# Kernel tuning notes

Hardware: AMD Instinct MI355X
Metric: run time of the kernel (lower is better)

## Reference

```python
import jax, jax.numpy as jnp
import numpy as np

N, IN_DIM, H, K = 4096, 64, 64, 3
DT = 0.05


def graph_filter(z, S_powers, W):
    # z: [N, d_in], S_powers: [K, N, N], W: [K, d_in, d_out]
    zk = jnp.einsum('knm,md->knd', S_powers, z)   # K-hop diffused features
    return jnp.einsum('knd,kde->ne', zk, W)       # sum over taps k


def setup_inputs() -> dict:
    key = jax.random.key(0)
    ks = jax.random.split(key, 8)
    w_scale = 0.1
    return {
        'x': jax.random.normal(ks[0], (N, H), jnp.float32),
        'u': jax.random.normal(ks[1], (N, IN_DIM), jnp.float32),
        'S_powers': jax.random.normal(ks[2], (K, N, N), jnp.float32) / np.float32(np.sqrt(N)),
        'WA_hat': jax.random.normal(ks[3], (K, H, H), jnp.float32) * w_scale,
        'WB_hat': jax.random.normal(ks[4], (K, IN_DIM, H), jnp.float32) * w_scale,
        'WA_state': jax.random.normal(ks[5], (K, H, H), jnp.float32) * w_scale,
        'WB_state': jax.random.normal(ks[6], (K, IN_DIM, H), jnp.float32) * w_scale,
        'bx': jnp.zeros((1, H), jnp.float32),
        'bu': jnp.zeros((1, H), jnp.float32),
        'b': jnp.ones((1, H), jnp.float32) * 0.1,
        'n_steps': 4,
    }


def reference(x, u, S_powers, WA_hat, WB_hat, WA_state, WB_state, bx, bu, b, n_steps):
    # Input-driven terms are constant across solver steps; hoist them.
    fu = jax.nn.relu(graph_filter(u, S_powers, WB_hat) + bu)   # [N, H]
    sigma_c = jnp.tanh(graph_filter(u, S_powers, WB_state))    # [N, H]

    def step(xc, _):
        f = jax.nn.relu(graph_filter(xc, S_powers, WA_hat) + bx) + fu
        dx = -(b + f) * xc - graph_filter(xc, S_powers, WA_state) + f * sigma_c
        xn = jnp.clip(xc + DT * dx, -1.0, 1.0)
        return xn, None

    xf, _ = jax.lax.scan(step, x, None, length=n_steps)
    return xf
```

## Files before the change

### kernel.cpp

```cpp
#include <hip/hip_runtime.h>
#include <math.h>


typedef unsigned short u16;
typedef unsigned int u32;
typedef __attribute__((ext_vector_type(8))) short short8;
typedef __attribute__((ext_vector_type(4))) float f32x4;

#define NN 4096
#define HD 64
#define KB32 128
#define DT_C 0.05f

__device__ __forceinline__ u16 f2bf(float f) {
    u32 u = __float_as_uint(f);
    u += 0x7FFFu + ((u >> 16) & 1u);
    return (u16)(u >> 16);
}
__device__ __forceinline__ u32 pk2(float a, float b) {
    return (u32)f2bf(a) | ((u32)f2bf(b) << 16);
}

__global__ __launch_bounds__(256) void convS_kernel(
    const float* __restrict__ S, u16* __restrict__ SbT)
{
    const int slab = blockIdx.y;
    const int tap = slab >> 7, kb = slab & 127;
    const int t = threadIdx.x;
    const int n = blockIdx.x * 64 + (t >> 2);
    const int kq = (t & 3) * 8;
    const float* src = S + ((size_t)tap * NN + n) * NN + kb * 32 + kq;
    float4 f0 = ((const float4*)src)[0];
    float4 f1 = ((const float4*)src)[1];
    uint4 o;
    o.x = pk2(f0.x, f0.y); o.y = pk2(f0.z, f0.w);
    o.z = pk2(f1.x, f1.y); o.w = pk2(f1.z, f1.w);
    *(uint4*)(SbT + ((size_t)slab * NN + n) * 32 + kq) = o;
}

__global__ __launch_bounds__(256) void zprep_kernel(
    const float* __restrict__ u, const float* __restrict__ x,
    const float* __restrict__ WAh, const float* __restrict__ WAs,
    const float* __restrict__ WBh, const float* __restrict__ WBs,
    u16* __restrict__ utT, u16* __restrict__ xtT, u16* __restrict__ WtT)
{
    const int b = blockIdx.x;
    const int t = threadIdx.x;
    if (b < 256) {
        const float* z = (b < 128) ? u : x;
        u16* ztT = (b < 128) ? utT : xtT;
        const int kb = b & 127, n0 = kb * 32;
        __shared__ __align__(16) u16 tile[64][40];
        const int nl = t >> 3, c0 = (t & 7) * 8;
        const float* src = z + (size_t)(n0 + nl) * HD + c0;
        float4 f0 = ((const float4*)src)[0];
        float4 f1 = ((const float4*)src)[1];
        tile[c0 + 0][nl] = f2bf(f0.x); tile[c0 + 1][nl] = f2bf(f0.y);
        tile[c0 + 2][nl] = f2bf(f0.z); tile[c0 + 3][nl] = f2bf(f0.w);
        tile[c0 + 4][nl] = f2bf(f1.x); tile[c0 + 5][nl] = f2bf(f1.y);
        tile[c0 + 6][nl] = f2bf(f1.z); tile[c0 + 7][nl] = f2bf(f1.w);
        __syncthreads();
        const int e = t >> 2, kw0 = (t & 3) * 8;
        short8 v = *(const short8*)&tile[e][kw0];
        *(short8*)(ztT + ((size_t)kb * 64 + e) * 32 + kw0) = v;
    } else {
        for (int f = t; f < 4 * 6 * 64 * 32; f += 256) {
            int mat = f / 12288, r = f % 12288;
            int s = r / 2048, r2 = r % 2048;
            int e = r2 >> 5, kw = r2 & 31;
            int kp = s * 32 + kw, tap = kp >> 6, d = kp & 63;
            const float* Wm = (mat == 0) ? WAh : (mat == 1) ? WAs : (mat == 2) ? WBh : WBs;
            WtT[f] = f2bf(Wm[((size_t)tap * HD + d) * HD + e]);
        }
    }
}

__global__ __launch_bounds__(256) void pack_kernel(
    const float* __restrict__ xn, u16* __restrict__ xtT)
{
    const int kb = blockIdx.x, n0 = kb * 32;
    const int t = threadIdx.x;
    __shared__ __align__(16) u16 tile[64][40];
    const int nl = t >> 3, c0 = (t & 7) * 8;
    const float* src = xn + (size_t)(n0 + nl) * HD + c0;
    float4 f0 = ((const float4*)src)[0];
    float4 f1 = ((const float4*)src)[1];
    tile[c0 + 0][nl] = f2bf(f0.x); tile[c0 + 1][nl] = f2bf(f0.y);
    tile[c0 + 2][nl] = f2bf(f0.z); tile[c0 + 3][nl] = f2bf(f0.w);
    tile[c0 + 4][nl] = f2bf(f1.x); tile[c0 + 5][nl] = f2bf(f1.y);
    tile[c0 + 6][nl] = f2bf(f1.z); tile[c0 + 7][nl] = f2bf(f1.w);
    __syncthreads();
    const int e = t >> 2, kw0 = (t & 3) * 8;
    short8 v = *(const short8*)&tile[e][kw0];
    *(short8*)(xtT + ((size_t)kb * 64 + e) * 32 + kw0) = v;
}

__global__ __launch_bounds__(256) void diffuseA_kernel(
    const u16* __restrict__ SbT, const u16* __restrict__ utT,
    const u16* __restrict__ xtT, float* __restrict__ Yp, int iters)
{
    const int t = threadIdx.x;
    const int tap = blockIdx.z;
    const int row0 = blockIdx.x * 128;
    const int kb0 = blockIdx.y * iters;
    const int w = t >> 6, lane = t & 63, l15 = lane & 15, quad = lane >> 4;

    const u16* A0 = SbT + (((size_t)(tap * KB32) * NN + row0 + w * 32 + l15) * 32) + quad * 8;
    const size_t arowstride = (size_t)NN * 32;
    const u16* Bu = utT + (size_t)(l15)*0;

    f32x4 z4 = {0.f, 0.f, 0.f, 0.f};
    f32x4 acc[2][2][4];
    #pragma unroll
    for (int s = 0; s < 2; ++s)
        #pragma unroll
        for (int i = 0; i < 2; ++i)
            #pragma unroll
            for (int j = 0; j < 4; ++j) acc[s][i][j] = z4;

    #pragma unroll 2
    for (int it = 0; it < iters; ++it) {
        const int kb = kb0 + it;
        const u16* ab = A0 + (size_t)kb * arowstride;
        short8 a0 = *(const short8*)(ab);
        short8 a1 = *(const short8*)(ab + 16 * 32);
        #pragma unroll
        for (int ct = 0; ct < 4; ++ct) {
            const size_t bo = ((size_t)kb * 64 + ct * 16 + l15) * 32 + quad * 8;
            short8 bu = *(const short8*)(utT + bo);
            short8 bx = *(const short8*)(xtT + bo);
            acc[0][0][ct] = __builtin_amdgcn_mfma_f32_16x16x32_bf16(a0, bu, acc[0][0][ct], 0, 0, 0);
            acc[0][1][ct] = __builtin_amdgcn_mfma_f32_16x16x32_bf16(a1, bu, acc[0][1][ct], 0, 0, 0);
            acc[1][0][ct] = __builtin_amdgcn_mfma_f32_16x16x32_bf16(a0, bx, acc[1][0][ct], 0, 0, 0);
            acc[1][1][ct] = __builtin_amdgcn_mfma_f32_16x16x32_bf16(a1, bx, acc[1][1][ct], 0, 0, 0);
        }
    }
    (void)Bu;
    #pragma unroll
    for (int s = 0; s < 2; ++s) {
        float* yb = Yp + ((size_t)((blockIdx.y * 3 + tap) * 2 + s) * NN + row0) * HD;
        #pragma unroll
        for (int rt = 0; rt < 2; ++rt)
            #pragma unroll
            for (int ct = 0; ct < 4; ++ct)
                #pragma unroll
                for (int r = 0; r < 4; ++r)
                    yb[(size_t)(w * 32 + rt * 16 + quad * 4 + r) * HD + ct * 16 + l15] = acc[s][rt][ct][r];
    }
}

__global__ __launch_bounds__(256) void diffuseS_kernel(
    const u16* __restrict__ SbT, const u16* __restrict__ xtT,
    float* __restrict__ Yp, int iters)
{
    const int t = threadIdx.x;
    const int tap = blockIdx.z;
    const int row0 = blockIdx.x * 128;
    const int kb0 = blockIdx.y * iters;
    const int w = t >> 6, lane = t & 63, l15 = lane & 15, quad = lane >> 4;

    const u16* A0 = SbT + (((size_t)(tap * KB32) * NN + row0 + w * 32 + l15) * 32) + quad * 8;
    const size_t arowstride = (size_t)NN * 32;

    f32x4 z4 = {0.f, 0.f, 0.f, 0.f};
    f32x4 acc[2][4];
    #pragma unroll
    for (int i = 0; i < 2; ++i)
        #pragma unroll
        for (int j = 0; j < 4; ++j) acc[i][j] = z4;

    #pragma unroll 2
    for (int it = 0; it < iters; ++it) {
        const int kb = kb0 + it;
        const u16* ab = A0 + (size_t)kb * arowstride;
        short8 a0 = *(const short8*)(ab);
        short8 a1 = *(const short8*)(ab + 16 * 32);
        #pragma unroll
        for (int ct = 0; ct < 4; ++ct) {
            short8 bb = *(const short8*)(xtT + ((size_t)kb * 64 + ct * 16 + l15) * 32 + quad * 8);
            acc[0][ct] = __builtin_amdgcn_mfma_f32_16x16x32_bf16(a0, bb, acc[0][ct], 0, 0, 0);
            acc[1][ct] = __builtin_amdgcn_mfma_f32_16x16x32_bf16(a1, bb, acc[1][ct], 0, 0, 0);
        }
    }
    float* yb = Yp + ((size_t)(blockIdx.y * 3 + tap) * NN + row0) * HD;
    #pragma unroll
    for (int rt = 0; rt < 2; ++rt)
        #pragma unroll
        for (int ct = 0; ct < 4; ++ct)
            #pragma unroll
            for (int r = 0; r < 4; ++r)
                yb[(size_t)(w * 32 + rt * 16 + quad * 4 + r) * HD + ct * 16 + l15] = acc[rt][ct][r];
}

__global__ __launch_bounds__(256) void reduce_kernel(
    const float* __restrict__ Yp, int KS, int nsrc,
    u16* __restrict__ dst0, u16* __restrict__ dst1)
{
    const int tg = blockIdx.x * 256 + threadIdx.x;
    const int src = tg / 98304;
    const int r = tg - src * 98304;
    const int tap = r >> 15;
    const int r2 = r & 32767;
    const int n = r2 >> 3;
    const int dg = (r2 & 7) * 8;
    const float* p = Yp + (((size_t)tap * nsrc + src) * NN + n) * HD + dg;
    const size_t kstride = (size_t)3 * nsrc * NN * HD;
    float4 s0 = {0.f, 0.f, 0.f, 0.f}, s1 = {0.f, 0.f, 0.f, 0.f};
    for (int ks = 0; ks < KS; ++ks) {
        float4 v0 = ((const float4*)(p + ks * kstride))[0];
        float4 v1 = ((const float4*)(p + ks * kstride))[1];
        s0.x += v0.x; s0.y += v0.y; s0.z += v0.z; s0.w += v0.w;
        s1.x += v1.x; s1.y += v1.y; s1.z += v1.z; s1.w += v1.w;
    }
    u16* dst = src ? dst1 : dst0;
    uint4 o;
    o.x = pk2(s0.x, s0.y); o.y = pk2(s0.z, s0.w);
    o.z = pk2(s1.x, s1.y); o.w = pk2(s1.z, s1.w);
    *(uint4*)(dst + (((size_t)(tap * 2 + (dg >> 5)) * NN + n) * 32) + (dg & 31)) = o;
}

__global__ __launch_bounds__(64) void update_step_kernel(
    const u16* __restrict__ YxT, const u16* __restrict__ WtT,
    const float* __restrict__ bx, const float* __restrict__ bvec,
    const float* __restrict__ fu, const float* __restrict__ sc,
    const float* __restrict__ xc, float* __restrict__ xn)
{
    const int n0 = blockIdx.x * 16;
    const int lane = threadIdx.x, l15 = lane & 15, quad = lane >> 4;

    f32x4 z4 = {0.f, 0.f, 0.f, 0.f};
    f32x4 aF[4], aG[4];
    #pragma unroll
    for (int ct = 0; ct < 4; ++ct) { aF[ct] = z4; aG[ct] = z4; }
    #pragma unroll
    for (int s = 0; s < 6; ++s) {
        short8 a = *(const short8*)(YxT + (((size_t)s * NN + n0 + l15) * 32) + quad * 8);
        #pragma unroll
        for (int ct = 0; ct < 4; ++ct) {
            const size_t wo = (((size_t)(0 * 6 + s) * 64) + ct * 16 + l15) * 32 + quad * 8;
            short8 bF = *(const short8*)(WtT + wo);
            short8 bG = *(const short8*)(WtT + wo + 6 * 64 * 32);
            aF[ct] = __builtin_amdgcn_mfma_f32_16x16x32_bf16(a, bF, aF[ct], 0, 0, 0);
            aG[ct] = __builtin_amdgcn_mfma_f32_16x16x32_bf16(a, bG, aG[ct], 0, 0, 0);
        }
    }
    #pragma unroll
    for (int ct = 0; ct < 4; ++ct) {
        const int e = ct * 16 + l15;
        const float bxv = bx[e], bbv = bvec[e];
        #pragma unroll
        for (int r = 0; r < 4; ++r) {
            const int n = n0 + quad * 4 + r;
            const size_t o = (size_t)n * HD + e;
            float f = fmaxf(aF[ct][r] + bxv, 0.f) + fu[o];
            float g = aG[ct][r];
            float xv = xc[o];
            float dx = -(bbv + f) * xv - g + f * sc[o];
            xn[o] = fminf(fmaxf(xv + DT_C * dx, -1.f), 1.f);
        }
    }
}

__global__ __launch_bounds__(64) void update1_kernel(
    const u16* __restrict__ YuT, const u16* __restrict__ YxT,
    const u16* __restrict__ WtT,
    const float* __restrict__ bx, const float* __restrict__ bu,
    const float* __restrict__ bvec, const float* __restrict__ x0,
    float* __restrict__ fu, float* __restrict__ sc, float* __restrict__ x1)
{
    const int n0 = blockIdx.x * 16;
    const int lane = threadIdx.x, l15 = lane & 15, quad = lane >> 4;

    f32x4 z4 = {0.f, 0.f, 0.f, 0.f};
    f32x4 aFu[4], aSc[4], aF[4], aG[4];
    #pragma unroll
    for (int ct = 0; ct < 4; ++ct) { aFu[ct] = z4; aSc[ct] = z4; aF[ct] = z4; aG[ct] = z4; }
    #pragma unroll
    for (int s = 0; s < 6; ++s) {
        const size_t ao = (((size_t)s * NN + n0 + l15) * 32) + quad * 8;
        short8 au = *(const short8*)(YuT + ao);
        short8 ax = *(const short8*)(YxT + ao);
        #pragma unroll
        for (int ct = 0; ct < 4; ++ct) {
            const size_t wo = (((size_t)s * 64) + ct * 16 + l15) * 32 + quad * 8;
            short8 bF  = *(const short8*)(WtT + wo);
            short8 bG  = *(const short8*)(WtT + wo + 6 * 64 * 32);
            short8 bFu = *(const short8*)(WtT + wo + 2 * 6 * 64 * 32);
            short8 bSc = *(const short8*)(WtT + wo + 3 * 6 * 64 * 32);
            aF[ct]  = __builtin_amdgcn_mfma_f32_16x16x32_bf16(ax, bF,  aF[ct],  0, 0, 0);
            aG[ct]  = __builtin_amdgcn_mfma_f32_16x16x32_bf16(ax, bG,  aG[ct],  0, 0, 0);
            aFu[ct] = __builtin_amdgcn_mfma_f32_16x16x32_bf16(au, bFu, aFu[ct], 0, 0, 0);
            aSc[ct] = __builtin_amdgcn_mfma_f32_16x16x32_bf16(au, bSc, aSc[ct], 0, 0, 0);
        }
    }
    #pragma unroll
    for (int ct = 0; ct < 4; ++ct) {
        const int e = ct * 16 + l15;
        const float bxv = bx[e], buv = bu[e], bbv = bvec[e];
        #pragma unroll
        for (int r = 0; r < 4; ++r) {
            const int n = n0 + quad * 4 + r;
            const size_t o = (size_t)n * HD + e;
            float fuv = fmaxf(aFu[ct][r] + buv, 0.f);
            float scv = tanhf(aSc[ct][r]);
            float f = fmaxf(aF[ct][r] + bxv, 0.f) + fuv;
            float g = aG[ct][r];
            float xv = x0[o];
            float dx = -(bbv + f) * xv - g + f * scv;
            fu[o] = fuv; sc[o] = scv;
            x1[o] = fminf(fmaxf(xv + DT_C * dx, -1.f), 1.f);
        }
    }
}

extern "C" void kernel_launch(void* const* d_in, const int* in_sizes, int n_in,
                              void* d_out, int out_size, void* d_ws, size_t ws_size,
                              hipStream_t stream) {
    const float* x   = (const float*)d_in[0];
    const float* u   = (const float*)d_in[1];
    const float* S   = (const float*)d_in[2];
    const float* WAh = (const float*)d_in[3];
    const float* WBh = (const float*)d_in[4];
    const float* WAs = (const float*)d_in[5];
    const float* WBs = (const float*)d_in[6];
    const float* bx  = (const float*)d_in[7];
    const float* bu  = (const float*)d_in[8];
    const float* bvec= (const float*)d_in[9];
    float* out = (float*)d_out;

    const size_t sbf_bytes = (size_t)3 * NN * NN * 2;
    const size_t slice = (size_t)NN * HD * 4;
    const size_t rest = 2 * 524288 + 98304 + 2 * 1572864 + 4 * 1048576;
    int KS_A = 4, KS_S = 8;
    if (ws_size < sbf_bytes + 24 * slice + rest) { KS_A = 2; KS_S = 4; }
    if (ws_size < sbf_bytes + 12 * slice + rest) { KS_A = 1; KS_S = 2; }
    const int nslice = (KS_A * 6 > KS_S * 3) ? KS_A * 6 : KS_S * 3;

    char* p = (char*)d_ws;
    u16* SbT  = (u16*)p;         p += sbf_bytes;
    float* Yp = (float*)p;       p += (size_t)nslice * slice;
    u16* utT  = (u16*)p;         p += 524288;
    u16* xtT  = (u16*)p;         p += 524288;
    u16* WtT  = (u16*)p;         p += 98304;
    u16* YuT  = (u16*)p;         p += 1572864;
    u16* YxT  = (u16*)p;         p += 1572864;
    float* fu = (float*)p;       p += 1048576;
    float* sc = (float*)p;       p += 1048576;
    float* xA = (float*)p;       p += 1048576;
    float* xB = (float*)p;       p += 1048576;

    zprep_kernel<<<257, 256, 0, stream>>>(u, x, WAh, WAs, WBh, WBs, utT, xtT, WtT);
    convS_kernel<<<dim3(64, 384), 256, 0, stream>>>(S, SbT);

    diffuseA_kernel<<<dim3(32, KS_A, 3), 256, 0, stream>>>(SbT, utT, xtT, Yp, KB32 / KS_A);
    reduce_kernel<<<768, 256, 0, stream>>>(Yp, KS_A, 2, YuT, YxT);
    update1_kernel<<<256, 64, 0, stream>>>(YuT, YxT, WtT, bx, bu, bvec, x, fu, sc, xA);
    pack_kernel<<<128, 256, 0, stream>>>(xA, xtT);
    diffuseS_kernel<<<dim3(32, KS_S, 3), 256, 0, stream>>>(SbT, xtT, Yp, KB32 / KS_S);
    reduce_kernel<<<384, 256, 0, stream>>>(Yp, KS_S, 1, YxT, YxT);
    update_step_kernel<<<256, 64, 0, stream>>>(YxT, WtT, bx, bvec, fu, sc, xA, xB);
    pack_kernel<<<128, 256, 0, stream>>>(xB, xtT);

    diffuseS_kernel<<<dim3(32, KS_S, 3), 256, 0, stream>>>(SbT, xtT, Yp, KB32 / KS_S);
    reduce_kernel<<<384, 256, 0, stream>>>(Yp, KS_S, 1, YxT, YxT);
    update_step_kernel<<<256, 64, 0, stream>>>(YxT, WtT, bx, bvec, fu, sc, xB, xA);
    pack_kernel<<<128, 256, 0, stream>>>(xA, xtT);

    diffuseS_kernel<<<dim3(32, KS_S, 3), 256, 0, stream>>>(SbT, xtT, Yp, KB32 / KS_S);
    reduce_kernel<<<384, 256, 0, stream>>>(Yp, KS_S, 1, YxT, YxT);
    update_step_kernel<<<256, 64, 0, stream>>>(YxT, WtT, bx, bvec, fu, sc, xA, out);
}
```

Before: 533.4 us.

## Fuse all stages into one cooperative persistent kernel with grid syncs

Replaces the chain of about sixteen kernel launches (conversion, diffusion, reduction, update, pack) with a single cooperative kernel of 256 persistent blocks that runs each phase in turn, separated by grid-wide syncs. The split-K partial sums are now reduced inside the update phase, and the update writes the bf16 transposed state directly, so the separate reduce and pack kernels are gone. The diffusion loops also gain explicit register double-buffering of the next K-block's operands. The aim is to remove launch gaps and intermediate round trips, at the cost of a fixed grid of one block per CU at 256 threads, which may limit latency hiding in the memory-bound S conversion and diffusion phases.

New measurement: 815.1 us. 52.8% more time.

```diff
diff --git a/kernel.cpp b/kernel.cpp
--- a/kernel.cpp
+++ b/kernel.cpp
@@ -1,5 +1,8 @@
 #include <hip/hip_runtime.h>
+#include <hip/hip_cooperative_groups.h>
 #include <math.h>
+
+namespace cg = cooperative_groups;
 
 
 typedef unsigned short u16;
@@ -9,7 +12,6 @@
 
 #define NN 4096
 #define HD 64
-#define KB32 128
 #define DT_C 0.05f
 
 __device__ __forceinline__ u16 f2bf(float f) {
@@ -20,353 +22,398 @@
 __device__ __forceinline__ u32 pk2(float a, float b) {
     return (u32)f2bf(a) | ((u32)f2bf(b) << 16);
 }
-
-__global__ __launch_bounds__(256) void convS_kernel(
-    const float* __restrict__ S, u16* __restrict__ SbT)
-{
-    const int slab = blockIdx.y;
-    const int tap = slab >> 7, kb = slab & 127;
-    const int t = threadIdx.x;
-    const int n = blockIdx.x * 64 + (t >> 2);
-    const int kq = (t & 3) * 8;
-    const float* src = S + ((size_t)tap * NN + n) * NN + kb * 32 + kq;
-    float4 f0 = ((const float4*)src)[0];
-    float4 f1 = ((const float4*)src)[1];
-    uint4 o;
-    o.x = pk2(f0.x, f0.y); o.y = pk2(f0.z, f0.w);
-    o.z = pk2(f1.x, f1.y); o.w = pk2(f1.z, f1.w);
-    *(uint4*)(SbT + ((size_t)slab * NN + n) * 32 + kq) = o;
-}
-
-__global__ __launch_bounds__(256) void zprep_kernel(
-    const float* __restrict__ u, const float* __restrict__ x,
-    const float* __restrict__ WAh, const float* __restrict__ WAs,
-    const float* __restrict__ WBh, const float* __restrict__ WBs,
-    u16* __restrict__ utT, u16* __restrict__ xtT, u16* __restrict__ WtT)
-{
-    const int b = blockIdx.x;
-    const int t = threadIdx.x;
-    if (b < 256) {
-        const float* z = (b < 128) ? u : x;
-        u16* ztT = (b < 128) ? utT : xtT;
-        const int kb = b & 127, n0 = kb * 32;
-        __shared__ __align__(16) u16 tile[64][40];
-        const int nl = t >> 3, c0 = (t & 7) * 8;
-        const float* src = z + (size_t)(n0 + nl) * HD + c0;
-        float4 f0 = ((const float4*)src)[0];
-        float4 f1 = ((const float4*)src)[1];
-        tile[c0 + 0][nl] = f2bf(f0.x); tile[c0 + 1][nl] = f2bf(f0.y);
-        tile[c0 + 2][nl] = f2bf(f0.z); tile[c0 + 3][nl] = f2bf(f0.w);
-        tile[c0 + 4][nl] = f2bf(f1.x); tile[c0 + 5][nl] = f2bf(f1.y);
-        tile[c0 + 6][nl] = f2bf(f1.z); tile[c0 + 7][nl] = f2bf(f1.w);
-        __syncthreads();
-        const int e = t >> 2, kw0 = (t & 3) * 8;
-        short8 v = *(const short8*)&tile[e][kw0];
-        *(short8*)(ztT + ((size_t)kb * 64 + e) * 32 + kw0) = v;
-    } else {
-        for (int f = t; f < 4 * 6 * 64 * 32; f += 256) {
-            int mat = f / 12288, r = f % 12288;
-            int s = r / 2048, r2 = r % 2048;
-            int e = r2 >> 5, kw = r2 & 31;
-            int kp = s * 32 + kw, tap = kp >> 6, d = kp & 63;
-            const float* Wm = (mat == 0) ? WAh : (mat == 1) ? WAs : (mat == 2) ? WBh : WBs;
-            WtT[f] = f2bf(Wm[((size_t)tap * HD + d) * HD + e]);
-        }
-    }
-}
-
-__global__ __launch_bounds__(256) void pack_kernel(
-    const float* __restrict__ xn, u16* __restrict__ xtT)
-{
-    const int kb = blockIdx.x, n0 = kb * 32;
+__device__ __forceinline__ short8 pkfrag(const float4& a, const float4& b) {
+    union { short8 s; u32 w[4]; } r;
+    r.w[0] = pk2(a.x, a.y); r.w[1] = pk2(a.z, a.w);
+    r.w[2] = pk2(b.x, b.y); r.w[3] = pk2(b.z, b.w);
+    return r.s;
+}
+__device__ __forceinline__ void add4(float4& d, const float4& v) {
+    d.x += v.x; d.y += v.y; d.z += v.z; d.w += v.w;
+}
+#define MFMA __builtin_amdgcn_mfma_f32_16x16x32_bf16
+
+__device__ void prep_phase(const float* S, const float* u, const float* x0,
+                           const float* WAh, const float* WAs,
+                           const float* WBh, const float* WBs,
+                           u16* SbT, u16* utT, u16* xtT, u16* WtT)
+{
     const int t = threadIdx.x;
     __shared__ __align__(16) u16 tile[64][40];
-    const int nl = t >> 3, c0 = (t & 7) * 8;
-    const float* src = xn + (size_t)(n0 + nl) * HD + c0;
-    float4 f0 = ((const float4*)src)[0];
-    float4 f1 = ((const float4*)src)[1];
-    tile[c0 + 0][nl] = f2bf(f0.x); tile[c0 + 1][nl] = f2bf(f0.y);
-    tile[c0 + 2][nl] = f2bf(f0.z); tile[c0 + 3][nl] = f2bf(f0.w);
-    tile[c0 + 4][nl] = f2bf(f1.x); tile[c0 + 5][nl] = f2bf(f1.y);
-    tile[c0 + 6][nl] = f2bf(f1.z); tile[c0 + 7][nl] = f2bf(f1.w);
-    __syncthreads();
-    const int e = t >> 2, kw0 = (t & 3) * 8;
-    short8 v = *(const short8*)&tile[e][kw0];
-    *(short8*)(xtT + ((size_t)kb * 64 + e) * 32 + kw0) = v;
-}
-
-__global__ __launch_bounds__(256) void diffuseA_kernel(
-    const u16* __restrict__ SbT, const u16* __restrict__ utT,
-    const u16* __restrict__ xtT, float* __restrict__ Yp, int iters)
+    for (int uu = blockIdx.x; uu < 24576 + 257; uu += 256) {
+        if (uu < 24576) {
+            const int nx = uu & 63, slab = uu >> 6;
+            const int tap = slab >> 7, kb = slab & 127;
+            const int n = nx * 64 + (t >> 2), kq = (t & 3) * 8;
+            const float* src = S + ((size_t)tap * NN + n) * NN + kb * 32 + kq;
+            float4 f0 = ((const float4*)src)[0];
+            float4 f1 = ((const float4*)src)[1];
+            uint4 o;
+            o.x = pk2(f0.x, f0.y); o.y = pk2(f0.z, f0.w);
+            o.z = pk2(f1.x, f1.y); o.w = pk2(f1.z, f1.w);
+            *(uint4*)(SbT + ((size_t)slab * NN + n) * 32 + kq) = o;
+        } else if (uu < 24832) {
+            const int zu = uu - 24576;
+            const float* z = (zu < 128) ? u : x0;
+            u16* ztT = (zu < 128) ? utT : xtT;
+            const int kb = zu & 127, n0 = kb * 32;
+            const int nl = t >> 3, c0 = (t & 7) * 8;
+            const float* srcz = z + (size_t)(n0 + nl) * HD + c0;
+            float4 f0 = ((const float4*)srcz)[0];
+            float4 f1 = ((const float4*)srcz)[1];
+            tile[c0 + 0][nl] = f2bf(f0.x); tile[c0 + 1][nl] = f2bf(f0.y);
+            tile[c0 + 2][nl] = f2bf(f0.z); tile[c0 + 3][nl] = f2bf(f0.w);
+            tile[c0 + 4][nl] = f2bf(f1.x); tile[c0 + 5][nl] = f2bf(f1.y);
+            tile[c0 + 6][nl] = f2bf(f1.z); tile[c0 + 7][nl] = f2bf(f1.w);
+            __syncthreads();
+            const int e = t >> 2, kw0 = (t & 3) * 8;
+            short8 v = *(const short8*)&tile[e][kw0];
+            *(short8*)(ztT + ((size_t)kb * 64 + e) * 32 + kw0) = v;
+            __syncthreads();
+        } else {
+            for (int f = t; f < 4 * 6 * 64 * 32; f += 256) {
+                int mat = f / 12288, r = f % 12288;
+                int s = r / 2048, r2 = r % 2048;
+                int e = r2 >> 5, kw = r2 & 31;
+                int kp = s * 32 + kw, tap = kp >> 6, d = kp & 63;
+                const float* Wm = (mat == 0) ? WAh : (mat == 1) ? WAs
+                                 : (mat == 2) ? WBh : WBs;
+                WtT[f] = f2bf(Wm[((size_t)tap * HD + d) * HD + e]);
+            }
+        }
+    }
+}
+
+__device__ void diffuse_step_phase(const u16* SbT, const u16* xtT,
+                                   float* Yp, int KS)
 {
     const int t = threadIdx.x;
-    const int tap = blockIdx.z;
-    const int row0 = blockIdx.x * 128;
-    const int kb0 = blockIdx.y * iters;
     const int w = t >> 6, lane = t & 63, l15 = lane & 15, quad = lane >> 4;
-
-    const u16* A0 = SbT + (((size_t)(tap * KB32) * NN + row0 + w * 32 + l15) * 32) + quad * 8;
-    const size_t arowstride = (size_t)NN * 32;
-    const u16* Bu = utT + (size_t)(l15)*0;
-
-    f32x4 z4 = {0.f, 0.f, 0.f, 0.f};
-    f32x4 acc[2][2][4];
-    #pragma unroll
-    for (int s = 0; s < 2; ++s)
+    const int iters = 128 / KS;
+    for (int uu = blockIdx.x; uu < 96 * KS; uu += 256) {
+        const int rowblk = uu & 31;
+        const int tmp = uu >> 5;
+        const int ks = tmp % KS, tap = tmp / KS;
+        const int row0 = rowblk * 128;
+        const int slab0 = tap * 128 + ks * iters;
+        const int kb0 = ks * iters;
+        const u16* A0 = SbT + ((size_t)slab0 * NN + row0 + w * 32 + l15) * 32 + quad * 8;
+        const u16* B0 = xtT + ((size_t)kb0 * 64 + l15) * 32 + quad * 8;
+
+        f32x4 z4 = {0.f, 0.f, 0.f, 0.f};
+        f32x4 acc[2][4];
         #pragma unroll
         for (int i = 0; i < 2; ++i)
             #pragma unroll
-            for (int j = 0; j < 4; ++j) acc[s][i][j] = z4;
-
-    #pragma unroll 2
-    for (int it = 0; it < iters; ++it) {
-        const int kb = kb0 + it;
-        const u16* ab = A0 + (size_t)kb * arowstride;
-        short8 a0 = *(const short8*)(ab);
-        short8 a1 = *(const short8*)(ab + 16 * 32);
-        #pragma unroll
-        for (int ct = 0; ct < 4; ++ct) {
-            const size_t bo = ((size_t)kb * 64 + ct * 16 + l15) * 32 + quad * 8;
-            short8 bu = *(const short8*)(utT + bo);
-            short8 bx = *(const short8*)(xtT + bo);
-            acc[0][0][ct] = __builtin_amdgcn_mfma_f32_16x16x32_bf16(a0, bu, acc[0][0][ct], 0, 0, 0);
-            acc[0][1][ct] = __builtin_amdgcn_mfma_f32_16x16x32_bf16(a1, bu, acc[0][1][ct], 0, 0, 0);
-            acc[1][0][ct] = __builtin_amdgcn_mfma_f32_16x16x32_bf16(a0, bx, acc[1][0][ct], 0, 0, 0);
-            acc[1][1][ct] = __builtin_amdgcn_mfma_f32_16x16x32_bf16(a1, bx, acc[1][1][ct], 0, 0, 0);
-        }
-    }
-    (void)Bu;
-    #pragma unroll
-    for (int s = 0; s < 2; ++s) {
-        float* yb = Yp + ((size_t)((blockIdx.y * 3 + tap) * 2 + s) * NN + row0) * HD;
+            for (int j = 0; j < 4; ++j) acc[i][j] = z4;
+
+        short8 a0 = *(const short8*)(A0);
+        short8 a1 = *(const short8*)(A0 + 512);
+        short8 b0 = *(const short8*)(B0);
+        short8 b1 = *(const short8*)(B0 + 512);
+        short8 b2 = *(const short8*)(B0 + 1024);
+        short8 b3 = *(const short8*)(B0 + 1536);
+        for (int kb = 1; kb < iters; ++kb) {
+            const u16* An = A0 + (size_t)kb * (NN * 32);
+            const u16* Bn = B0 + (size_t)kb * 2048;
+            short8 na0 = *(const short8*)(An);
+            short8 na1 = *(const short8*)(An + 512);
+            short8 nb0 = *(const short8*)(Bn);
+            short8 nb1 = *(const short8*)(Bn + 512);
+            short8 nb2 = *(const short8*)(Bn + 1024);
+            short8 nb3 = *(const short8*)(Bn + 1536);
+            acc[0][0] = MFMA(a0, b0, acc[0][0], 0, 0, 0);
+            acc[1][0] = MFMA(a1, b0, acc[1][0], 0, 0, 0);
+            acc[0][1] = MFMA(a0, b1, acc[0][1], 0, 0, 0);
+            acc[1][1] = MFMA(a1, b1, acc[1][1], 0, 0, 0);
+            acc[0][2] = MFMA(a0, b2, acc[0][2], 0, 0, 0);
+            acc[1][2] = MFMA(a1, b2, acc[1][2], 0, 0, 0);
+            acc[0][3] = MFMA(a0, b3, acc[0][3], 0, 0, 0);
+            acc[1][3] = MFMA(a1, b3, acc[1][3], 0, 0, 0);
+            a0 = na0; a1 = na1; b0 = nb0; b1 = nb1; b2 = nb2; b3 = nb3;
+        }
+        acc[0][0] = MFMA(a0, b0, acc[0][0], 0, 0, 0);
+        acc[1][0] = MFMA(a1, b0, acc[1][0], 0, 0, 0);
+        acc[0][1] = MFMA(a0, b1, acc[0][1], 0, 0, 0);
+        acc[1][1] = MFMA(a1, b1, acc[1][1], 0, 0, 0);
+        acc[0][2] = MFMA(a0, b2, acc[0][2], 0, 0, 0);
+        acc[1][2] = MFMA(a1, b2, acc[1][2], 0, 0, 0);
+        acc[0][3] = MFMA(a0, b3, acc[0][3], 0, 0, 0);
+        acc[1][3] = MFMA(a1, b3, acc[1][3], 0, 0, 0);
+
+        float* yb = Yp + ((size_t)(ks * 3 + tap) * NN + row0) * HD;
         #pragma unroll
         for (int rt = 0; rt < 2; ++rt)
             #pragma unroll
             for (int ct = 0; ct < 4; ++ct)
                 #pragma unroll
                 for (int r = 0; r < 4; ++r)
-                    yb[(size_t)(w * 32 + rt * 16 + quad * 4 + r) * HD + ct * 16 + l15] = acc[s][rt][ct][r];
-    }
-}
-
-__global__ __launch_bounds__(256) void diffuseS_kernel(
-    const u16* __restrict__ SbT, const u16* __restrict__ xtT,
-    float* __restrict__ Yp, int iters)
+                    yb[(size_t)(w * 32 + rt * 16 + quad * 4 + r) * HD + ct * 16 + l15] =
+                        acc[rt][ct][r];
+    }
+}
+
+__device__ void diffuseA_phase(const u16* SbT, const u16* utT, const u16* xtT,
+                               float* Yp, int KS)
 {
     const int t = threadIdx.x;
-    const int tap = blockIdx.z;
-    const int row0 = blockIdx.x * 128;
-    const int kb0 = blockIdx.y * iters;
     const int w = t >> 6, lane = t & 63, l15 = lane & 15, quad = lane >> 4;
-
-    const u16* A0 = SbT + (((size_t)(tap * KB32) * NN + row0 + w * 32 + l15) * 32) + quad * 8;
-    const size_t arowstride = (size_t)NN * 32;
-
-    f32x4 z4 = {0.f, 0.f, 0.f, 0.f};
-    f32x4 acc[2][4];
-    #pragma unroll
-    for (int i = 0; i < 2; ++i)
+    const int iters = 128 / KS;
+    for (int uu = blockIdx.x; uu < 96 * KS; uu += 256) {
+        const int rowblk = uu & 31;
+        const int tmp = uu >> 5;
+        const int ks = tmp % KS, tap = tmp / KS;
+        const int row0 = rowblk * 128;
+        const int slab0 = tap * 128 + ks * iters;
+        const int kb0 = ks * iters;
+        const u16* A0 = SbT + ((size_t)slab0 * NN + row0 + w * 32 + l15) * 32 + quad * 8;
+        const size_t boff = ((size_t)kb0 * 64 + l15) * 32 + quad * 8;
+
+        f32x4 z4 = {0.f, 0.f, 0.f, 0.f};
+        f32x4 acc[2][2][4];
         #pragma unroll
-        for (int j = 0; j < 4; ++j) acc[i][j] = z4;
-
-    #pragma unroll 2
-    for (int it = 0; it < iters; ++it) {
-        const int kb = kb0 + it;
-        const u16* ab = A0 + (size_t)kb * arowstride;
-        short8 a0 = *(const short8*)(ab);
-        short8 a1 = *(const short8*)(ab + 16 * 32);
+        for (int s = 0; s < 2; ++s)
+            #pragma unroll
+            for (int i = 0; i < 2; ++i)
+                #pragma unroll
+                for (int j = 0; j < 4; ++j) acc[s][i][j] = z4;
+
+        short8 a0 = *(const short8*)(A0);
+        short8 a1 = *(const short8*)(A0 + 512);
+        short8 bu0 = *(const short8*)(utT + boff);
+        short8 bu1 = *(const short8*)(utT + boff + 512);
+        short8 bu2 = *(const short8*)(utT + boff + 1024);
+        short8 bu3 = *(const short8*)(utT + boff + 1536);
+        short8 bx0 = *(const short8*)(xtT + boff);
+        short8 bx1 = *(const short8*)(xtT + boff + 512);
+        short8 bx2 = *(const short8*)(xtT + boff + 1024);
+        short8 bx3 = *(const short8*)(xtT + boff + 1536);
+        for (int kb = 1; kb < iters; ++kb) {
+            const u16* An = A0 + (size_t)kb * (NN * 32);
+            const size_t bn = boff + (size_t)kb * 2048;
+            short8 na0 = *(const short8*)(An);
+            short8 na1 = *(const short8*)(An + 512);
+            short8 nu0 = *(const short8*)(utT + bn);
+            short8 nu1 = *(const short8*)(utT + bn + 512);
+            short8 nu2 = *(const short8*)(utT + bn + 1024);
+            short8 nu3 = *(const short8*)(utT + bn + 1536);
+            short8 nx0 = *(const short8*)(xtT + bn);
+            short8 nx1 = *(const short8*)(xtT + bn + 512);
+            short8 nx2 = *(const short8*)(xtT + bn + 1024);
+            short8 nx3 = *(const short8*)(xtT + bn + 1536);
+            acc[0][0][0] = MFMA(a0, bu0, acc[0][0][0], 0, 0, 0);
+            acc[0][1][0] = MFMA(a1, bu0, acc[0][1][0], 0, 0, 0);
+            acc[0][0][1] = MFMA(a0, bu1, acc[0][0][1], 0, 0, 0);
+            acc[0][1][1] = MFMA(a1, bu1, acc[0][1][1], 0, 0, 0);
+            acc[0][0][2] = MFMA(a0, bu2, acc[0][0][2], 0, 0, 0);
+            acc[0][1][2] = MFMA(a1, bu2, acc[0][1][2], 0, 0, 0);
+            acc[0][0][3] = MFMA(a0, bu3, acc[0][0][3], 0, 0, 0);
+            acc[0][1][3] = MFMA(a1, bu3, acc[0][1][3], 0, 0, 0);
+            acc[1][0][0] = MFMA(a0, bx0, acc[1][0][0], 0, 0, 0);
+            acc[1][1][0] = MFMA(a1, bx0, acc[1][1][0], 0, 0, 0);
+            acc[1][0][1] = MFMA(a0, bx1, acc[1][0][1], 0, 0, 0);
+            acc[1][1][1] = MFMA(a1, bx1, acc[1][1][1], 0, 0, 0);
+            acc[1][0][2] = MFMA(a0, bx2, acc[1][0][2], 0, 0, 0);
+            acc[1][1][2] = MFMA(a1, bx2, acc[1][1][2], 0, 0, 0);
+            acc[1][0][3] = MFMA(a0, bx3, acc[1][0][3], 0, 0, 0);
+            acc[1][1][3] = MFMA(a1, bx3, acc[1][1][3], 0, 0, 0);
+            a0 = na0; a1 = na1;
+            bu0 = nu0; bu1 = nu1; bu2 = nu2; bu3 = nu3;
+            bx0 = nx0; bx1 = nx1; bx2 = nx2; bx3 = nx3;
+        }
+        acc[0][0][0] = MFMA(a0, bu0, acc[0][0][0], 0, 0, 0);
+        acc[0][1][0] = MFMA(a1, bu0, acc[0][1][0], 0, 0, 0);
+        acc[0][0][1] = MFMA(a0, bu1, acc[0][0][1], 0, 0, 0);
+        acc[0][1][1] = MFMA(a1, bu1, acc[0][1][1], 0, 0, 0);
+        acc[0][0][2] = MFMA(a0, bu2, acc[0][0][2], 0, 0, 0);
+        acc[0][1][2] = MFMA(a1, bu2, acc[0][1][2], 0, 0, 0);
+        acc[0][0][3] = MFMA(a0, bu3, acc[0][0][3], 0, 0, 0);
+        acc[0][1][3] = MFMA(a1, bu3, acc[0][1][3], 0, 0, 0);
+        acc[1][0][0] = MFMA(a0, bx0, acc[1][0][0], 0, 0, 0);
+        acc[1][1][0] = MFMA(a1, bx0, acc[1][1][0], 0, 0, 0);
+        acc[1][0][1] = MFMA(a0, bx1, acc[1][0][1], 0, 0, 0);
+        acc[1][1][1] = MFMA(a1, bx1, acc[1][1][1], 0, 0, 0);
+        acc[1][0][2] = MFMA(a0, bx2, acc[1][0][2], 0, 0, 0);
+        acc[1][1][2] = MFMA(a1, bx2, acc[1][1][2], 0, 0, 0);
+        acc[1][0][3] = MFMA(a0, bx3, acc[1][0][3], 0, 0, 0);
+        acc[1][1][3] = MFMA(a1, bx3, acc[1][1][3], 0, 0, 0);
+
         #pragma unroll
-        for (int ct = 0; ct < 4; ++ct) {
-            short8 bb = *(const short8*)(xtT + ((size_t)kb * 64 + ct * 16 + l15) * 32 + quad * 8);
-            acc[0][ct] = __builtin_amdgcn_mfma_f32_16x16x32_bf16(a0, bb, acc[0][ct], 0, 0, 0);
-            acc[1][ct] = __builtin_amdgcn_mfma_f32_16x16x32_bf16(a1, bb, acc[1][ct], 0, 0, 0);
-        }
-    }
-    float* yb = Yp + ((size_t)(blockIdx.y * 3 + tap) * NN + row0) * HD;
-    #pragma unroll
-    for (int rt = 0; rt < 2; ++rt)
-        #pragma unroll
-        for (int ct = 0; ct < 4; ++ct)
+        for (int s = 0; s < 2; ++s) {
+            float* yb = Yp + ((size_t)((ks * 3 + tap) * 2 + s) * NN + row0) * HD;
             #pragma unroll
-            for (int r = 0; r < 4; ++r)
-                yb[(size_t)(w * 32 + rt * 16 + quad * 4 + r) * HD + ct * 16 + l15] = acc[rt][ct][r];
-}
-
-__global__ __launch_bounds__(256) void reduce_kernel(
-    const float* __restrict__ Yp, int KS, int nsrc,
-    u16* __restrict__ dst0, u16* __restrict__ dst1)
-{
-    const int tg = blockIdx.x * 256 + threadIdx.x;
-    const int src = tg / 98304;
-    const int r = tg - src * 98304;
-    const int tap = r >> 15;
-    const int r2 = r & 32767;
-    const int n = r2 >> 3;
-    const int dg = (r2 & 7) * 8;
-    const float* p = Yp + (((size_t)tap * nsrc + src) * NN + n) * HD + dg;
-    const size_t kstride = (size_t)3 * nsrc * NN * HD;
-    float4 s0 = {0.f, 0.f, 0.f, 0.f}, s1 = {0.f, 0.f, 0.f, 0.f};
-    for (int ks = 0; ks < KS; ++ks) {
-        float4 v0 = ((const float4*)(p + ks * kstride))[0];
-        float4 v1 = ((const float4*)(p + ks * kstride))[1];
-        s0.x += v0.x; s0.y += v0.y; s0.z += v0.z; s0.w += v0.w;
-        s1.x += v1.x; s1.y += v1.y; s1.z += v1.z; s1.w += v1.w;
-    }
-    u16* dst = src ? dst1 : dst0;
-    uint4 o;
-    o.x = pk2(s0.x, s0.y); o.y = pk2(s0.z, s0.w);
-    o.z = pk2(s1.x, s1.y); o.w = pk2(s1.z, s1.w);
-    *(uint4*)(dst + (((size_t)(tap * 2 + (dg >> 5)) * NN + n) * 32) + (dg & 31)) = o;
-}
-
-__global__ __launch_bounds__(64) void update_step_kernel(
-    const u16* __restrict__ YxT, const u16* __restrict__ WtT,
-    const float* __restrict__ bx, const float* __restrict__ bvec,
-    const float* __restrict__ fu, const float* __restrict__ sc,
-    const float* __restrict__ xc, float* __restrict__ xn)
-{
+            for (int rt = 0; rt < 2; ++rt)
+                #pragma unroll
+                for (int ct = 0; ct < 4; ++ct)
+                    #pragma unroll
+                    for (int r = 0; r < 4; ++r)
+                        yb[(size_t)(w * 32 + rt * 16 + quad * 4 + r) * HD + ct * 16 + l15] =
+                            acc[s][rt][ct][r];
+        }
+    }
+}
+
+__device__ void update_step_phase(const float* Yp, int KS, const u16* WtT,
+                                  const float* bx, const float* bvec,
+                                  const float* fu, const float* sc,
+                                  const float* xc, float* xn, u16* xtT)
+{
+    const int t = threadIdx.x;
+    const int w = t >> 6, lane = t & 63, l15 = lane & 15, quad = lane >> 4;
     const int n0 = blockIdx.x * 16;
-    const int lane = threadIdx.x, l15 = lane & 15, quad = lane >> 4;
-
-    f32x4 z4 = {0.f, 0.f, 0.f, 0.f};
-    f32x4 aF[4], aG[4];
-    #pragma unroll
-    for (int ct = 0; ct < 4; ++ct) { aF[ct] = z4; aG[ct] = z4; }
+    f32x4 aF = {0.f, 0.f, 0.f, 0.f}, aG = aF;
     #pragma unroll
     for (int s = 0; s < 6; ++s) {
-        short8 a = *(const short8*)(YxT + (((size_t)s * NN + n0 + l15) * 32) + quad * 8);
-        #pragma unroll
-        for (int ct = 0; ct < 4; ++ct) {
-            const size_t wo = (((size_t)(0 * 6 + s) * 64) + ct * 16 + l15) * 32 + quad * 8;
-            short8 bF = *(const short8*)(WtT + wo);
-            short8 bG = *(const short8*)(WtT + wo + 6 * 64 * 32);
-            aF[ct] = __builtin_amdgcn_mfma_f32_16x16x32_bf16(a, bF, aF[ct], 0, 0, 0);
-            aG[ct] = __builtin_amdgcn_mfma_f32_16x16x32_bf16(a, bG, aG[ct], 0, 0, 0);
-        }
-    }
+        const float* base = Yp + ((size_t)(s >> 1) * NN + n0 + l15) * HD
+                               + (s & 1) * 32 + quad * 8;
+        float4 p0 = {0.f, 0.f, 0.f, 0.f}, p1 = p0;
+        for (int ks = 0; ks < KS; ++ks) {
+            const float* pp = base + (size_t)ks * 3 * NN * HD;
+            add4(p0, ((const float4*)pp)[0]);
+            add4(p1, ((const float4*)pp)[1]);
+        }
+        short8 a = pkfrag(p0, p1);
+        const size_t wo = ((size_t)s * 64 + w * 16 + l15) * 32 + quad * 8;
+        short8 bF = *(const short8*)(WtT + wo);
+        short8 bG = *(const short8*)(WtT + wo + 12288);
+        aF = MFMA(a, bF, aF, 0, 0, 0);
+        aG = MFMA(a, bG, aG, 0, 0, 0);
+    }
+    const int e = w * 16 + l15;
+    const float bxv = bx[e], bbv = bvec[e];
     #pragma unroll
-    for (int ct = 0; ct < 4; ++ct) {
-        const int e = ct * 16 + l15;
-        const float bxv = bx[e], bbv = bvec[e];
-        #pragma unroll
-        for (int r = 0; r < 4; ++r) {
-            const int n = n0 + quad * 4 + r;
-            const size_t o = (size_t)n * HD + e;
-            float f = fmaxf(aF[ct][r] + bxv, 0.f) + fu[o];
-            float g = aG[ct][r];
-            float xv = xc[o];
-            float dx = -(bbv + f) * xv - g + f * sc[o];
-            xn[o] = fminf(fmaxf(xv + DT_C * dx, -1.f), 1.f);
-        }
-    }
-}
-
-__global__ __launch_bounds__(64) void update1_kernel(
-    const u16* __restrict__ YuT, const u16* __restrict__ YxT,
-    const u16* __restrict__ WtT,
-    const float* __restrict__ bx, const float* __restrict__ bu,
-    const float* __restrict__ bvec, const float* __restrict__ x0,
-    float* __restrict__ fu, float* __restrict__ sc, float* __restrict__ x1)
-{
+    for (int r = 0; r < 4; ++r) {
+        const int n = n0 + quad * 4 + r;
+        const size_t o = (size_t)n * HD + e;
+        float f = fmaxf(aF[r] + bxv, 0.f) + fu[o];
+        float xv = xc[o];
+        float dx = -(bbv + f) * xv - aG[r] + f * sc[o];
+        float xnv = fminf(fmaxf(xv + DT_C * dx, -1.f), 1.f);
+        xn[o] = xnv;
+        xtT[((size_t)(n >> 5) * 64 + e) * 32 + (n & 31)] = f2bf(xnv);
+    }
+}
+
+__device__ void update1_phase(const float* Yp, int KS, const u16* WtT,
+                              const float* bx, const float* bu, const float* bvec,
+                              const float* x0, float* fu, float* sc,
+                              float* xn, u16* xtT)
+{
+    const int t = threadIdx.x;
+    const int w = t >> 6, lane = t & 63, l15 = lane & 15, quad = lane >> 4;
     const int n0 = blockIdx.x * 16;
-    const int lane = threadIdx.x, l15 = lane & 15, quad = lane >> 4;
-
-    f32x4 z4 = {0.f, 0.f, 0.f, 0.f};
-    f32x4 aFu[4], aSc[4], aF[4], aG[4];
-    #pragma unroll
-    for (int ct = 0; ct < 4; ++ct) { aFu[ct] = z4; aSc[ct] = z4; aF[ct] = z4; aG[ct] = z4; }
+    f32x4 aF = {0.f, 0.f, 0.f, 0.f}, aG = aF, aFu = aF, aSc = aF;
     #pragma unroll
     for (int s = 0; s < 6; ++s) {
-        const size_t ao = (((size_t)s * NN + n0 + l15) * 32) + quad * 8;
-        short8 au = *(const short8*)(YuT + ao);
-        short8 ax = *(const short8*)(YxT + ao);
-        #pragma unroll
-        for (int ct = 0; ct < 4; ++ct) {
-            const size_t wo = (((size_t)s * 64) + ct * 16 + l15) * 32 + quad * 8;
-            short8 bF  = *(const short8*)(WtT + wo);
-            short8 bG  = *(const short8*)(WtT + wo + 6 * 64 * 32);
-            short8 bFu = *(const short8*)(WtT + wo + 2 * 6 * 64 * 32);
-            short8 bSc = *(const short8*)(WtT + wo + 3 * 6 * 64 * 32);
-            aF[ct]  = __builtin_amdgcn_mfma_f32_16x16x32_bf16(ax, bF,  aF[ct],  0, 0, 0);
-            aG[ct]  = __builtin_amdgcn_mfma_f32_16x16x32_bf16(ax, bG,  aG[ct],  0, 0, 0);
-            aFu[ct] = __builtin_amdgcn_mfma_f32_16x16x32_bf16(au, bFu, aFu[ct], 0, 0, 0);
-            aSc[ct] = __builtin_amdgcn_mfma_f32_16x16x32_bf16(au, bSc, aSc[ct], 0, 0, 0);
-        }
-    }
+        const float* baseu = Yp + ((size_t)((s >> 1) * 2 + 0) * NN + n0 + l15) * HD
+                                + (s & 1) * 32 + quad * 8;
+        const float* basex = baseu + (size_t)NN * HD;
+        float4 pu0 = {0.f, 0.f, 0.f, 0.f}, pu1 = pu0, px0 = pu0, px1 = pu0;
+        for (int ks = 0; ks < KS; ++ks) {
+            const float* ppu = baseu + (size_t)ks * 6 * NN * HD;
+            const float* ppx = basex + (size_t)ks * 6 * NN * HD;
+            add4(pu0, ((const float4*)ppu)[0]);
+            add4(pu1, ((const float4*)ppu)[1]);
+            add4(px0, ((const float4*)ppx)[0]);
+            add4(px1, ((const float4*)ppx)[1]);
+        }
+        short8 au = pkfrag(pu0, pu1);
+        short8 ax = pkfrag(px0, px1);
+        const size_t wo = ((size_t)s * 64 + w * 16 + l15) * 32 + quad * 8;
+        short8 bF  = *(const short8*)(WtT + wo);
+        short8 bG  = *(const short8*)(WtT + wo + 12288);
+        short8 bFu = *(const short8*)(WtT + wo + 24576);
+        short8 bSc = *(const short8*)(WtT + wo + 36864);
+        aF  = MFMA(ax, bF,  aF,  0, 0, 0);
+        aG  = MFMA(ax, bG,  aG,  0, 0, 0);
+        aFu = MFMA(au, bFu, aFu, 0, 0, 0);
+        aSc = MFMA(au, bSc, aSc, 0, 0, 0);
+    }
+    const int e = w * 16 + l15;
+    const float bxv = bx[e], buv = bu[e], bbv = bvec[e];
     #pragma unroll
-    for (int ct = 0; ct < 4; ++ct) {
-        const int e = ct * 16 + l15;
-        const float bxv = bx[e], buv = bu[e], bbv = bvec[e];
-        #pragma unroll
-        for (int r = 0; r < 4; ++r) {
-            const int n = n0 + quad * 4 + r;
-            const size_t o = (size_t)n * HD + e;
-            float fuv = fmaxf(aFu[ct][r] + buv, 0.f);
-            float scv = tanhf(aSc[ct][r]);
-            float f = fmaxf(aF[ct][r] + bxv, 0.f) + fuv;
-            float g = aG[ct][r];
-            float xv = x0[o];
-            float dx = -(bbv + f) * xv - g + f * scv;
-            fu[o] = fuv; sc[o] = scv;
-            x1[o] = fminf(fmaxf(xv + DT_C * dx, -1.f), 1.f);
-        }
-    }
+    for (int r = 0; r < 4; ++r) {
+        const int n = n0 + quad * 4 + r;
+        const size_t o = (size_t)n * HD + e;
+        float fuv = fmaxf(aFu[r] + buv, 0.f);
+        float scv = tanhf(aSc[r]);
+        float f = fmaxf(aF[r] + bxv, 0.f) + fuv;
+        float xv = x0[o];
+        float dx = -(bbv + f) * xv - aG[r] + f * scv;
+        float xnv = fminf(fmaxf(xv + DT_C * dx, -1.f), 1.f);
+        fu[o] = fuv; sc[o] = scv; xn[o] = xnv;
+        xtT[((size_t)(n >> 5) * 64 + e) * 32 + (n & 31)] = f2bf(xnv);
+    }
+}
+
+__global__ __launch_bounds__(256, 1) void lgtcn_kernel(
+    const float* x0, const float* u, const float* S,
+    const float* WAh, const float* WBh, const float* WAs, const float* WBs,
+    const float* bx, const float* bu, const float* bvec,
+    u16* SbT, u16* utT, u16* xtT, u16* WtT,
+    float* Yp, float* fu, float* sc, float* xA, float* xB, float* out,
+    int KS)
+{
+    cg::grid_group grid = cg::this_grid();
+
+    prep_phase(S, u, x0, WAh, WAs, WBh, WBs, SbT, utT, xtT, WtT);
+    grid.sync();
+
+    diffuseA_phase(SbT, utT, xtT, Yp, KS);
+    grid.sync();
+    update1_phase(Yp, KS, WtT, bx, bu, bvec, x0, fu, sc, xA, xtT);
+    grid.sync();
+
+    diffuse_step_phase(SbT, xtT, Yp, KS);
+    grid.sync();
+    update_step_phase(Yp, KS, WtT, bx, bvec, fu, sc, xA, xB, xtT);
+    grid.sync();
+
+    diffuse_step_phase(SbT, xtT, Yp, KS);
+    grid.sync();
+    update_step_phase(Yp, KS, WtT, bx, bvec, fu, sc, xB, xA, xtT);
+    grid.sync();
+
+    diffuse_step_phase(SbT, xtT, Yp, KS);
+    grid.sync();
+    update_step_phase(Yp, KS, WtT, bx, bvec, fu, sc, xA, out, xtT);
 }
 
 extern "C" void kernel_launch(void* const* d_in, const int* in_sizes, int n_in,
                               void* d_out, int out_size, void* d_ws, size_t ws_size,
                               hipStream_t stream) {
-    const float* x   = (const float*)d_in[0];
-    const float* u   = (const float*)d_in[1];
-    const float* S   = (const float*)d_in[2];
-    const float* WAh = (const float*)d_in[3];
-    const float* WBh = (const float*)d_in[4];
-    const float* WAs = (const float*)d_in[5];
-    const float* WBs = (const float*)d_in[6];
-    const float* bx  = (const float*)d_in[7];
-    const float* bu  = (const float*)d_in[8];
-    const float* bvec= (const float*)d_in[9];
+    float* x   = (float*)d_in[0];
+    float* u   = (float*)d_in[1];
+    float* S   = (float*)d_in[2];
+    float* WAh = (float*)d_in[3];
+    float* WBh = (float*)d_in[4];
+    float* WAs = (float*)d_in[5];
+    float* WBs = (float*)d_in[6];
+    float* bx  = (float*)d_in[7];
+    float* bu  = (float*)d_in[8];
+    float* bvec= (float*)d_in[9];
     float* out = (float*)d_out;
 
-    const size_t sbf_bytes = (size_t)3 * NN * NN * 2;
-    const size_t slice = (size_t)NN * HD * 4;
-    const size_t rest = 2 * 524288 + 98304 + 2 * 1572864 + 4 * 1048576;
-    int KS_A = 4, KS_S = 8;
-    if (ws_size < sbf_bytes + 24 * slice + rest) { KS_A = 2; KS_S = 4; }
-    if (ws_size < sbf_bytes + 12 * slice + rest) { KS_A = 1; KS_S = 2; }
-    const int nslice = (KS_A * 6 > KS_S * 3) ? KS_A * 6 : KS_S * 3;
+    const size_t sbf = (size_t)3 * NN * NN * 2;
+    const size_t small = 2 * 524288 + 98304 + 4 * (size_t)NN * HD * 4;
+    int KS = 8;
+    while (KS > 1 && ws_size < sbf + (size_t)KS * 6 * NN * HD * 4 + small) KS >>= 1;
 
     char* p = (char*)d_ws;
-    u16* SbT  = (u16*)p;         p += sbf_bytes;
-    float* Yp = (float*)p;       p += (size_t)nslice * slice;
-    u16* utT  = (u16*)p;         p += 524288;
-    u16* xtT  = (u16*)p;         p += 524288;
-    u16* WtT  = (u16*)p;         p += 98304;
-    u16* YuT  = (u16*)p;         p += 1572864;
-    u16* YxT  = (u16*)p;         p += 1572864;
-    float* fu = (float*)p;       p += 1048576;
-    float* sc = (float*)p;       p += 1048576;
-    float* xA = (float*)p;       p += 1048576;
-    float* xB = (float*)p;       p += 1048576;
-
-    zprep_kernel<<<257, 256, 0, stream>>>(u, x, WAh, WAs, WBh, WBs, utT, xtT, WtT);
-    convS_kernel<<<dim3(64, 384), 256, 0, stream>>>(S, SbT);
-
-    diffuseA_kernel<<<dim3(32, KS_A, 3), 256, 0, stream>>>(SbT, utT, xtT, Yp, KB32 / KS_A);
-    reduce_kernel<<<768, 256, 0, stream>>>(Yp, KS_A, 2, YuT, YxT);
-    update1_kernel<<<256, 64, 0, stream>>>(YuT, YxT, WtT, bx, bu, bvec, x, fu, sc, xA);
-    pack_kernel<<<128, 256, 0, stream>>>(xA, xtT);
-    diffuseS_kernel<<<dim3(32, KS_S, 3), 256, 0, stream>>>(SbT, xtT, Yp, KB32 / KS_S);
-    reduce_kernel<<<384, 256, 0, stream>>>(Yp, KS_S, 1, YxT, YxT);
-    update_step_kernel<<<256, 64, 0, stream>>>(YxT, WtT, bx, bvec, fu, sc, xA, xB);
-    pack_kernel<<<128, 256, 0, stream>>>(xB, xtT);
-
-    diffuseS_kernel<<<dim3(32, KS_S, 3), 256, 0, stream>>>(SbT, xtT, Yp, KB32 / KS_S);
-    reduce_kernel<<<384, 256, 0, stream>>>(Yp, KS_S, 1, YxT, YxT);
-    update_step_kernel<<<256, 64, 0, stream>>>(YxT, WtT, bx, bvec, fu, sc, xB, xA);
-    pack_kernel<<<128, 256, 0, stream>>>(xA, xtT);
-
-    diffuseS_kernel<<<dim3(32, KS_S, 3), 256, 0, stream>>>(SbT, xtT, Yp, KB32 / KS_S);
-    reduce_kernel<<<384, 256, 0, stream>>>(Yp, KS_S, 1, YxT, YxT);
-    update_step_kernel<<<256, 64, 0, stream>>>(YxT, WtT, bx, bvec, fu, sc, xA, out);
-}
+    u16* SbT  = (u16*)p;   p += sbf;
+    float* Yp = (float*)p; p += (size_t)KS * 6 * NN * HD * 4;
+    u16* utT  = (u16*)p;   p += 524288;
+    u16* xtT  = (u16*)p;   p += 524288;
+    u16* WtT  = (u16*)p;   p += 98304;
+    float* fu = (float*)p; p += (size_t)NN * HD * 4;
+    float* sc = (float*)p; p += (size_t)NN * HD * 4;
+    float* xA = (float*)p; p += (size_t)NN * HD * 4;
+    float* xB = (float*)p; p += (size_t)NN * HD * 4;
+
+    void* args[] = {
+        &x, &u, &S, &WAh, &WBh, &WAs, &WBs, &bx, &bu, &bvec,
+        &SbT, &utT, &xtT, &WtT, &Yp, &fu, &sc, &xA, &xB, &out, &KS
+    };
+    hipLaunchCooperativeKernel((const void*)lgtcn_kernel,
+                               dim3(256), dim3(256), args, 0, stream);
+}
```
